# Kernel tuning notes

Hardware: AMD Instinct MI355X
Metric: run time of the kernel (lower is better)

The kernel has to match this reference:

```python
import jax, jax.numpy as jnp
import numpy as np
import math

NUM_BUCKETS = 32
MAX_DISTANCE = 128
N_HEADS = 16
D_KV = 64


def _relative_position_bucket(relative_position, num_buckets=NUM_BUCKETS, max_distance=MAX_DISTANCE):
    # bidirectional (encoder) variant
    num_buckets //= 2
    relative_buckets = (relative_position > 0).astype(jnp.int32) * num_buckets
    rp = jnp.abs(relative_position)
    max_exact = num_buckets // 2
    is_small = rp < max_exact
    rp_large = max_exact + (
        jnp.log(jnp.maximum(rp, 1).astype(jnp.float32) / max_exact)
        / math.log(max_distance / max_exact)
        * (num_buckets - max_exact)
    ).astype(jnp.int32)
    rp_large = jnp.minimum(rp_large, num_buckets - 1)
    return relative_buckets + jnp.where(is_small, rp, rp_large)


def compute_bias(rel_bias, q_len, k_len):
    ctx = jnp.arange(q_len)[:, None]
    mem = jnp.arange(k_len)[None, :]
    buckets = _relative_position_bucket(mem - ctx)          # [q, k]
    values = rel_bias[buckets]                               # [q, k, h]
    return jnp.transpose(values, (2, 0, 1))[None]            # [1, h, q, k]


def setup_inputs() -> dict:
    key = jax.random.key(0)
    ks = jax.random.split(key, 6)
    d_model, inner = 1024, N_HEADS * D_KV
    s = 0.02
    return {
        "hidden_states": jax.random.normal(ks[0], (2, 2048, d_model), jnp.float32),
        "Wq": jax.random.normal(ks[1], (d_model, inner), jnp.float32) * s,
        "Wk": jax.random.normal(ks[2], (d_model, inner), jnp.float32) * s,
        "Wv": jax.random.normal(ks[3], (d_model, inner), jnp.float32) * s,
        "Wo": jax.random.normal(ks[4], (inner, d_model), jnp.float32) * s,
        "rel_bias": jax.random.normal(ks[5], (NUM_BUCKETS, N_HEADS), jnp.float32) * s,
    }


def reference(hidden_states, Wq, Wk, Wv, Wo, rel_bias):
    B, S, D = hidden_states.shape

    def split_heads(x):  # [B,S,inner] -> [B,H,S,dk]
        return x.reshape(B, S, N_HEADS, D_KV).transpose(0, 2, 1, 3)

    q = split_heads(hidden_states @ Wq)
    k = split_heads(hidden_states @ Wk)
    v = split_heads(hidden_states @ Wv)

    # T5 does NOT scale by 1/sqrt(d_kv)
    scores = jnp.einsum("bhqd,bhkd->bhqk", q, k)
    scores = scores + compute_bias(rel_bias, S, S)
    attn = jax.nn.softmax(scores, axis=-1)
    ctx = jnp.einsum("bhqk,bhkd->bhqd", attn, v)
    ctx = ctx.transpose(0, 2, 1, 3).reshape(B, S, N_HEADS * D_KV)
    return ctx @ Wo
```

## Files before the change

kernel.cpp:

```cpp
#include <hip/hip_runtime.h>
#include <hip/hip_bf16.h>

typedef __bf16 bf16x8 __attribute__((ext_vector_type(8)));
typedef __bf16 bf16x4 __attribute__((ext_vector_type(4)));
typedef float floatx4 __attribute__((ext_vector_type(4)));
typedef float floatx16 __attribute__((ext_vector_type(16)));
using bf16 = __hip_bfloat16;

#define S_    2048
#define NHEAD 16
#define LOG2E 1.4426950408889634f

__device__ __forceinline__ void load_lds16(const bf16* g, void* lds) {
  __builtin_amdgcn_global_load_lds((const __attribute__((address_space(1))) void*)g,
                                   (__attribute__((address_space(3))) void*)lds, 16, 0, 0);
}

__global__ void prep_kernel(const float* __restrict__ hidden,
                            const float* __restrict__ wq, const float* __restrict__ wk,
                            const float* __restrict__ wv, const float* __restrict__ wo,
                            const float* __restrict__ rel_bias,
                            bf16* __restrict__ hbf, bf16* __restrict__ wt_qkv,
                            bf16* __restrict__ wt_o, float* __restrict__ tab) {
  __shared__ bf16 tile[32][33];
  int bid = blockIdx.x;
  if (bid < 4096) {
    int i = (bid * 256 + threadIdx.x) * 4;
    float4 v = *(const float4*)(hidden + i);
    bf16 o[4] = {__float2bfloat16(v.x), __float2bfloat16(v.y),
                 __float2bfloat16(v.z), __float2bfloat16(v.w)};
    *(uint2*)(hbf + i) = *(const uint2*)o;
  } else if (bid < 8192) {
    int r = bid - 4096;
    int mat = r >> 10;
    int rem = r & 1023;
    int n0 = (rem & 31) * 32, k0 = (rem >> 5) * 32;
    int tx = threadIdx.x & 31, ty = threadIdx.x >> 5;
    const float* src = (mat == 0) ? wq : (mat == 1) ? wk : (mat == 2) ? wv : wo;
    bf16* dst = (mat == 3) ? wt_o : wt_qkv + mat * 1024 * 1024;
#pragma unroll
    for (int j = 0; j < 32; j += 8)
      tile[ty + j][tx] = __float2bfloat16(src[(k0 + ty + j) * 1024 + n0 + tx]);
    __syncthreads();
#pragma unroll
    for (int j = 0; j < 32; j += 8)
      dst[(n0 + ty + j) * 1024 + k0 + tx] = tile[tx][ty + j];
  } else {
    int idx = (bid - 8192) * 256 + threadIdx.x;
    int h = idx >> 12, j = idx & 4095;
    int delta = j - 2048;
    int rb = (delta > 0) ? 16 : 0;
    int rpa = delta < 0 ? -delta : delta;
    int bsmall;
    if (rpa < 8) {
      bsmall = rpa;
    } else {
      int lg = 25 - __clz(rpa * rpa);
      bsmall = 8 + lg;
      if (bsmall > 15) bsmall = 15;
    }
    tab[idx] = rel_bias[(rb + bsmall) * 16 + h] * LOG2E;
  }
}

__global__ __launch_bounds__(512) void gemm_qkv_kernel(const bf16* __restrict__ A,
                                                       const bf16* __restrict__ Bt,
                                                       bf16* __restrict__ qh,
                                                       bf16* __restrict__ kf,
                                                       bf16* __restrict__ vf) {
  const int K = 1024;
  __shared__ char lds[131072];
  int t = threadIdx.x;
  int m0 = blockIdx.y * 256, n0 = blockIdx.x * 256;
  int w = t >> 6, lane = t & 63, ln = lane & 15, quad = lane >> 4;
  int wm = w >> 2, wn = w & 3;
  floatx4 acc[8][4];
  floatx4 zero = {0.f, 0.f, 0.f, 0.f};
#pragma unroll
  for (int i = 0; i < 8; i++)
#pragma unroll
    for (int j = 0; j < 4; j++) acc[i][j] = zero;

  int r = t >> 3, c8 = t & 7;
  int cs = (c8 ^ (r & 7)) * 8;
  const bf16* Ag = A + (long)(m0 + r) * K + cs;
  const bf16* Bg = Bt + (long)(n0 + r) * K + cs;

#define QKV_STAGE(bufi, kt)                                                     \
  {                                                                             \
    char* ab = lds + (bufi) * 65536;                                            \
    char* bb = ab + 32768;                                                      \
    int kk = (kt) * 64;                                                         \
    _Pragma("unroll")                                                           \
    for (int ch = 0; ch < 4; ch++) {                                            \
      load_lds16(Ag + (long)ch * 64 * K + kk, ab + ch * 8192 + t * 16);         \
      load_lds16(Bg + (long)ch * 64 * K + kk, bb + ch * 8192 + t * 16);         \
    }                                                                           \
  }

  QKV_STAGE(0, 0);
  QKV_STAGE(1, 1);
  asm volatile("s_waitcnt vmcnt(8)" ::: "memory");
  __builtin_amdgcn_s_barrier();

  for (int kt = 0; kt < 16; ++kt) {
    const bf16* As_ = (const bf16*)(lds + (kt & 1) * 65536);
    const bf16* Bs_ = As_ + 16384;
#pragma unroll
    for (int s = 0; s < 2; s++) {
      int slot = ((s * 4 + quad) ^ (ln & 7)) * 8;
      bf16x8 af[8], bfv[4];
#pragma unroll
      for (int i = 0; i < 8; i++)
        af[i] = *(const bf16x8*)&As_[(wm * 128 + i * 16 + ln) * 64 + slot];
#pragma unroll
      for (int j = 0; j < 4; j++)
        bfv[j] = *(const bf16x8*)&Bs_[(wn * 64 + j * 16 + ln) * 64 + slot];
      __builtin_amdgcn_s_setprio(1);
#pragma unroll
      for (int i = 0; i < 8; i++)
#pragma unroll
        for (int j = 0; j < 4; j++)
          acc[i][j] = __builtin_amdgcn_mfma_f32_16x16x32_bf16(af[i], bfv[j], acc[i][j], 0, 0, 0);
      __builtin_amdgcn_s_setprio(0);
    }
    if (kt == 15) break;
    __builtin_amdgcn_s_barrier();
    if (kt + 2 < 16) {
      QKV_STAGE(kt & 1, kt + 2);
      asm volatile("s_waitcnt vmcnt(8)" ::: "memory");
    } else {
      asm volatile("s_waitcnt vmcnt(0)" ::: "memory");
    }
    __builtin_amdgcn_s_barrier();
  }
#undef QKV_STAGE

  int nb = n0 + wn * 64;
  int type = nb >> 10, h = (nb >> 6) & 15;
  int b = (m0 >> 11);
  int sl0 = (m0 & 2047) + wm * 128;
  long bhbase = (long)((b * 16 + h)) * 131072;

  if (type == 0) {
#pragma unroll
    for (int i = 0; i < 8; i++)
#pragma unroll
      for (int j = 0; j < 4; j++) {
        int d = j * 16 + ln;
#pragma unroll
        for (int rr = 0; rr < 4; rr++) {
          int s = sl0 + i * 16 + quad * 4 + rr;
          qh[bhbase + (long)s * 64 + d] = __float2bfloat16(acc[i][j][rr]);
        }
      }
  } else if (type == 1) {
#pragma unroll
    for (int i = 0; i < 8; i++)
#pragma unroll
      for (int j = 0; j < 4; j++) {
        long base = bhbase + sl0 * 64 + (i >> 1) * 2048 + j * 512 + (ln >> 3) * 256 +
                    (i & 1) * 128 + quad * 32 + (ln & 7);
#pragma unroll
        for (int rr = 0; rr < 4; rr++)
          kf[base + rr * 8] = __float2bfloat16(acc[i][j][rr]);
      }
  } else {
#pragma unroll
    for (int i = 0; i < 8; i++)
#pragma unroll
      for (int j = 0; j < 4; j++) {
        long off = sl0 * 64 + i * 1024 + (j >> 1) * 512 + (quad >> 1) * 256 +
                   ((j & 1) * 16 + ln) * 8 + (quad & 1) * 4;
        bf16x4 pk = {(__bf16)acc[i][j][0], (__bf16)acc[i][j][1],
                     (__bf16)acc[i][j][2], (__bf16)acc[i][j][3]};
        *(bf16x4*)(vf + bhbase + off) = pk;
      }
  }
}

#define LOADKV(Kr, Vr, kk)                                        \
  {                                                               \
    const bf16* kp = kfb + (kk) * 64 + loff;                      \
    const bf16* vp = vfb + (kk) * 64 + loff;                      \
    Kr[0] = *(const bf16x8*)(kp);                                 \
    Kr[1] = *(const bf16x8*)(kp + 512);                           \
    Kr[2] = *(const bf16x8*)(kp + 1024);                          \
    Kr[3] = *(const bf16x8*)(kp + 1536);                          \
    Vr[0] = *(const bf16x8*)(vp);                                 \
    Vr[1] = *(const bf16x8*)(vp + 512);                           \
    Vr[2] = *(const bf16x8*)(vp + 1024);                          \
    Vr[3] = *(const bf16x8*)(vp + 1536);                          \
  }

#define COMPUTE(Kr, Vr, kk)                                                       \
  {                                                                               \
    floatx16 st = zf;                                                             \
    __builtin_amdgcn_s_setprio(1);                                                \
    st = __builtin_amdgcn_mfma_f32_32x32x16_bf16(Kr[0], Qf[0], st, 0, 0, 0);      \
    st = __builtin_amdgcn_mfma_f32_32x32x16_bf16(Kr[1], Qf[1], st, 0, 0, 0);      \
    st = __builtin_amdgcn_mfma_f32_32x32x16_bf16(Kr[2], Qf[2], st, 0, 0, 0);      \
    st = __builtin_amdgcn_mfma_f32_32x32x16_bf16(Kr[3], Qf[3], st, 0, 0, 0);      \
    __builtin_amdgcn_s_setprio(0);                                                \
    float p[16];                                                                  \
    bool near = ((kk) > qw - 160) && ((kk) < qw + 160);                           \
    if (near) {                                                                   \
      int kb = (kk) + 4 * h5 - (qw + l31) + 2048;                                 \
      _Pragma("unroll")                                                           \
      for (int r = 0; r < 16; r++)                                                \
        p[r] = __builtin_amdgcn_exp2f(                                            \
            fmaf(st[r], LOG2E, bt[kb + (r & 3) + 8 * (r >> 2)]));                 \
    } else {                                                                      \
      float cb = ((kk) > qw) ? cpos : cneg;                                       \
      _Pragma("unroll")                                                           \
      for (int r = 0; r < 16; r++)                                                \
        p[r] = __builtin_amdgcn_exp2f(fmaf(st[r], LOG2E, cb));                    \
    }                                                                             \
    float a0 = (p[0] + p[1]) + (p[2] + p[3]);                                     \
    float a1 = (p[4] + p[5]) + (p[6] + p[7]);                                     \
    float a2 = (p[8] + p[9]) + (p[10] + p[11]);                                   \
    float a3 = (p[12] + p[13]) + (p[14] + p[15]);                                 \
    l_acc += (a0 + a1) + (a2 + a3);                                               \
    unsigned d[8];                                                                \
    _Pragma("unroll")                                                             \
    for (int i = 0; i < 8; i++)                                                   \
      asm("v_cvt_pk_bf16_f32 %0, %1, %2" : "=v"(d[i]) : "v"(p[2*i]), "v"(p[2*i+1])); \
    unsigned w0 = d[0], w2 = d[2];                                                \
    asm("v_permlane32_swap_b32 %0, %1" : "+v"(w0), "+v"(w2));                     \
    unsigned w1 = d[1], w3 = d[3];                                                \
    asm("v_permlane32_swap_b32 %0, %1" : "+v"(w1), "+v"(w3));                     \
    unsigned w4 = d[4], w6 = d[6];                                                \
    asm("v_permlane32_swap_b32 %0, %1" : "+v"(w4), "+v"(w6));                     \
    unsigned w5 = d[5], w7 = d[7];                                                \
    asm("v_permlane32_swap_b32 %0, %1" : "+v"(w5), "+v"(w7));                     \
    union { unsigned u[4]; bf16x8 v; } a0u, a1u;                                  \
    a0u.u[0] = w0; a0u.u[1] = w1; a0u.u[2] = w2; a0u.u[3] = w3;                   \
    a1u.u[0] = w4; a1u.u[1] = w5; a1u.u[2] = w6; a1u.u[3] = w7;                   \
    __builtin_amdgcn_s_setprio(1);                                                \
    o0 = __builtin_amdgcn_mfma_f32_32x32x16_bf16(a0u.v, Vr[0], o0, 0, 0, 0);      \
    o1 = __builtin_amdgcn_mfma_f32_32x32x16_bf16(a0u.v, Vr[1], o1, 0, 0, 0);      \
    o0 = __builtin_amdgcn_mfma_f32_32x32x16_bf16(a1u.v, Vr[2], o0, 0, 0, 0);      \
    o1 = __builtin_amdgcn_mfma_f32_32x32x16_bf16(a1u.v, Vr[3], o1, 0, 0, 0);      \
    __builtin_amdgcn_s_setprio(0);                                                \
  }

__global__ __launch_bounds__(256, 2) void attn_kernel(const bf16* __restrict__ qh,
                                                      const bf16* __restrict__ kf,
                                                      const bf16* __restrict__ vf,
                                                      const float* __restrict__ btab,
                                                      bf16* __restrict__ ctx) {
  int t = threadIdx.x, w = t >> 6, lane = t & 63;
  int l31 = lane & 31, h5 = lane >> 5;

  int lin = blockIdx.x;
  int xcd = lin & 7, j = lin >> 3;
  int bh = xcd * 4 + (j >> 4);
  int qblk = j & 15;
  int b = bh >> 4, h = bh & 15;
  int qw = qblk * 128 + w * 32;

  const bf16* qbase = qh + (long)bh * S_ * 64;
  const bf16* kfb = kf + (long)bh * S_ * 64;
  const bf16* vfb = vf + (long)bh * S_ * 64;
  const float* bt = btab + h * 4096;
  int loff = h5 * 256 + l31 * 8;

  bf16x8 Qf[4];
#pragma unroll
  for (int ds = 0; ds < 4; ds++)
    Qf[ds] = *(const bf16x8*)(qbase + (long)(qw + l31) * 64 + ds * 16 + h5 * 8);

  float cneg = bt[0], cpos = bt[4095];
  float l_acc = 0.f;
  floatx16 zf = {0.f, 0.f, 0.f, 0.f, 0.f, 0.f, 0.f, 0.f,
                 0.f, 0.f, 0.f, 0.f, 0.f, 0.f, 0.f, 0.f};
  floatx16 o0 = zf, o1 = zf;

  bf16x8 Ka[4], Va[4], Kb[4], Vb[4];
  LOADKV(Ka, Va, 0);
  LOADKV(Kb, Vb, 32);

  for (int k0 = 0; k0 < S_; k0 += 64) {
    COMPUTE(Ka, Va, k0);
    if (k0 + 64 < S_) LOADKV(Ka, Va, k0 + 64);
    COMPUTE(Kb, Vb, k0 + 32);
    if (k0 + 96 < S_) LOADKV(Kb, Vb, k0 + 96);
  }

  l_acc += __shfl_xor(l_acc, 32);
  float linv = 1.0f / l_acc;
#pragma unroll
  for (int r = 0; r < 16; r++) {
    int qrow = (r & 3) + 8 * (r >> 2) + 4 * h5;
    float lv = __shfl(linv, qrow);
    int q = qw + qrow;
    long base = (long)(b * S_ + q) * 1024 + h * 64 + l31;
    ctx[base] = __float2bfloat16(o0[r] * lv);
    ctx[base + 32] = __float2bfloat16(o1[r] * lv);
  }
}

__global__ __launch_bounds__(256) void gemm_bt_kernel(const bf16* __restrict__ A,
                                                      const bf16* __restrict__ Bt,
                                                      float* __restrict__ C,
                                                      int M, int N, int K) {
  __shared__ bf16 As[64 * 32];
  __shared__ bf16 Bs[128 * 32];
  int t = threadIdx.x;
  int m0 = blockIdx.y * 64, n0 = blockIdx.x * 128;
  int w = t >> 6, lane = t & 63, ln = lane & 15, quad = lane >> 4;
  int wr = w & 1, wc = w >> 1;
  floatx4 acc[2][4];
  floatx4 zero = {0.f, 0.f, 0.f, 0.f};
#pragma unroll
  for (int i = 0; i < 2; i++)
#pragma unroll
    for (int j = 0; j < 4; j++) acc[i][j] = zero;

  int r = t >> 2, c = (t & 3) * 8;
  const bf16* Ag = A + (long)(m0 + r) * K + c;
  const bf16* Bg = Bt + (long)(n0 + r) * K + c;
  char* ldsA0 = (char*)As + w * 1024;
  char* ldsB0 = (char*)Bs + w * 1024;
  char* ldsB1 = ldsB0 + 4096;

  for (int k0 = 0; k0 < K; k0 += 32) {
    load_lds16(Ag + k0, ldsA0);
    load_lds16(Bg + k0, ldsB0);
    load_lds16(Bg + (long)64 * K + k0, ldsB1);
    __syncthreads();
    bf16x8 af[2], bfv[4];
#pragma unroll
    for (int i = 0; i < 2; i++)
      af[i] = *(const bf16x8*)&As[(wr * 32 + i * 16 + ln) * 32 + quad * 8];
#pragma unroll
    for (int j = 0; j < 4; j++)
      bfv[j] = *(const bf16x8*)&Bs[(wc * 64 + j * 16 + ln) * 32 + quad * 8];
#pragma unroll
    for (int i = 0; i < 2; i++)
#pragma unroll
      for (int j = 0; j < 4; j++)
        acc[i][j] = __builtin_amdgcn_mfma_f32_16x16x32_bf16(af[i], bfv[j], acc[i][j], 0, 0, 0);
    __syncthreads();
  }

#pragma unroll
  for (int i = 0; i < 2; i++)
#pragma unroll
    for (int j = 0; j < 4; j++)
#pragma unroll
      for (int rr = 0; rr < 4; rr++)
        C[(long)(m0 + wr * 32 + i * 16 + quad * 4 + rr) * N + n0 + wc * 64 + j * 16 + ln] =
            acc[i][j][rr];
}

extern "C" void kernel_launch(void* const* d_in, const int* in_sizes, int n_in,
                              void* d_out, int out_size, void* d_ws, size_t ws_size,
                              hipStream_t stream) {
  (void)in_sizes; (void)n_in; (void)out_size; (void)ws_size;
  const float* hidden   = (const float*)d_in[0];
  const float* Wq       = (const float*)d_in[1];
  const float* Wk       = (const float*)d_in[2];
  const float* Wv       = (const float*)d_in[3];
  const float* Wo       = (const float*)d_in[4];
  const float* rel_bias = (const float*)d_in[5];

  char* ws = (char*)d_ws;
  bf16*  hbf    = (bf16*)(ws + 0);
  bf16*  wt_qkv = (bf16*)(ws + 8388608);
  bf16*  wt_o   = (bf16*)(ws + 14680064);
  float* btab   = (float*)(ws + 16777216);
  bf16*  qh     = (bf16*)(ws + 17039360);
  bf16*  kf     = (bf16*)(ws + 25427968);
  bf16*  vf     = (bf16*)(ws + 33816576);
  bf16*  ctx    = (bf16*)(ws + 42205184);

  prep_kernel<<<dim3(8448), dim3(256), 0, stream>>>(hidden, Wq, Wk, Wv, Wo, rel_bias,
                                                    hbf, wt_qkv, wt_o, btab);
  gemm_qkv_kernel<<<dim3(12, 16), dim3(512), 0, stream>>>(hbf, wt_qkv, qh, kf, vf);
  attn_kernel<<<dim3(512), dim3(256), 0, stream>>>(qh, kf, vf, btab, ctx);
  gemm_bt_kernel<<<dim3(8, 64), dim3(256), 0, stream>>>(ctx, wt_o, (float*)d_out, 4096, 1024, 1024);
}
```

Before: 187.8 us.

## Double-buffer output GEMM loads, enlarge weight transpose tiles, reuse workspace for ctx

```diff
diff --git a/kernel.cpp b/kernel.cpp
--- a/kernel.cpp
+++ b/kernel.cpp
@@ -22,7 +22,7 @@
                             const float* __restrict__ rel_bias,
                             bf16* __restrict__ hbf, bf16* __restrict__ wt_qkv,
                             bf16* __restrict__ wt_o, float* __restrict__ tab) {
-  __shared__ bf16 tile[32][33];
+  __shared__ bf16 tile[64][65];
   int bid = blockIdx.x;
   if (bid < 4096) {
     int i = (bid * 256 + threadIdx.x) * 4;
@@ -30,23 +30,23 @@
     bf16 o[4] = {__float2bfloat16(v.x), __float2bfloat16(v.y),
                  __float2bfloat16(v.z), __float2bfloat16(v.w)};
     *(uint2*)(hbf + i) = *(const uint2*)o;
-  } else if (bid < 8192) {
+  } else if (bid < 5120) {
     int r = bid - 4096;
-    int mat = r >> 10;
-    int rem = r & 1023;
-    int n0 = (rem & 31) * 32, k0 = (rem >> 5) * 32;
-    int tx = threadIdx.x & 31, ty = threadIdx.x >> 5;
+    int mat = r >> 8;
+    int rem = r & 255;
+    int n0 = (rem & 15) * 64, k0 = (rem >> 4) * 64;
+    int tx = threadIdx.x & 63, ty = threadIdx.x >> 6;
     const float* src = (mat == 0) ? wq : (mat == 1) ? wk : (mat == 2) ? wv : wo;
     bf16* dst = (mat == 3) ? wt_o : wt_qkv + mat * 1024 * 1024;
 #pragma unroll
-    for (int j = 0; j < 32; j += 8)
+    for (int j = 0; j < 64; j += 4)
       tile[ty + j][tx] = __float2bfloat16(src[(k0 + ty + j) * 1024 + n0 + tx]);
     __syncthreads();
 #pragma unroll
-    for (int j = 0; j < 32; j += 8)
+    for (int j = 0; j < 64; j += 4)
       dst[(n0 + ty + j) * 1024 + k0 + tx] = tile[tx][ty + j];
   } else {
-    int idx = (bid - 8192) * 256 + threadIdx.x;
+    int idx = (bid - 5120) * 256 + threadIdx.x;
     int h = idx >> 12, j = idx & 4095;
     int delta = j - 2048;
     int rb = (delta > 0) ? 16 : 0;
@@ -304,8 +304,7 @@
                                                       const bf16* __restrict__ Bt,
                                                       float* __restrict__ C,
                                                       int M, int N, int K) {
-  __shared__ bf16 As[64 * 32];
-  __shared__ bf16 Bs[128 * 32];
+  __shared__ char lds[2][12288];
   int t = threadIdx.x;
   int m0 = blockIdx.y * 64, n0 = blockIdx.x * 128;
   int w = t >> 6, lane = t & 63, ln = lane & 15, quad = lane >> 4;
@@ -320,29 +319,49 @@
   int r = t >> 2, c = (t & 3) * 8;
   const bf16* Ag = A + (long)(m0 + r) * K + c;
   const bf16* Bg = Bt + (long)(n0 + r) * K + c;
-  char* ldsA0 = (char*)As + w * 1024;
-  char* ldsB0 = (char*)Bs + w * 1024;
-  char* ldsB1 = ldsB0 + 4096;
-
-  for (int k0 = 0; k0 < K; k0 += 32) {
-    load_lds16(Ag + k0, ldsA0);
-    load_lds16(Bg + k0, ldsB0);
-    load_lds16(Bg + (long)64 * K + k0, ldsB1);
-    __syncthreads();
+
+#define BT_STAGE(bufi, kt)                                                      \
+  {                                                                             \
+    int kk = (kt) * 32;                                                         \
+    char* base = lds[bufi] + w * 1024;                                          \
+    load_lds16(Ag + kk, base);                                                  \
+    load_lds16(Bg + kk, base + 4096);                                           \
+    load_lds16(Bg + (long)64 * K + kk, base + 8192);                            \
+  }
+
+  BT_STAGE(0, 0);
+  BT_STAGE(1, 1);
+  asm volatile("s_waitcnt vmcnt(3)" ::: "memory");
+  __builtin_amdgcn_s_barrier();
+
+  for (int kt = 0; kt < 32; ++kt) {
+    const bf16* As_ = (const bf16*)lds[kt & 1];
+    const bf16* Bs_ = As_ + 2048;
     bf16x8 af[2], bfv[4];
 #pragma unroll
     for (int i = 0; i < 2; i++)
-      af[i] = *(const bf16x8*)&As[(wr * 32 + i * 16 + ln) * 32 + quad * 8];
+      af[i] = *(const bf16x8*)&As_[(wr * 32 + i * 16 + ln) * 32 + quad * 8];
 #pragma unroll
     for (int j = 0; j < 4; j++)
-      bfv[j] = *(const bf16x8*)&Bs[(wc * 64 + j * 16 + ln) * 32 + quad * 8];
+      bfv[j] = *(const bf16x8*)&Bs_[(wc * 64 + j * 16 + ln) * 32 + quad * 8];
+    __builtin_amdgcn_s_setprio(1);
 #pragma unroll
     for (int i = 0; i < 2; i++)
 #pragma unroll
       for (int j = 0; j < 4; j++)
         acc[i][j] = __builtin_amdgcn_mfma_f32_16x16x32_bf16(af[i], bfv[j], acc[i][j], 0, 0, 0);
-    __syncthreads();
-  }
+    __builtin_amdgcn_s_setprio(0);
+    if (kt == 31) break;
+    __builtin_amdgcn_s_barrier();
+    if (kt + 2 < 32) {
+      BT_STAGE(kt & 1, kt + 2);
+      asm volatile("s_waitcnt vmcnt(3)" ::: "memory");
+    } else {
+      asm volatile("s_waitcnt vmcnt(0)" ::: "memory");
+    }
+    __builtin_amdgcn_s_barrier();
+  }
+#undef BT_STAGE
 
 #pragma unroll
   for (int i = 0; i < 2; i++)
@@ -373,9 +392,9 @@
   bf16*  qh     = (bf16*)(ws + 17039360);
   bf16*  kf     = (bf16*)(ws + 25427968);
   bf16*  vf     = (bf16*)(ws + 33816576);
-  bf16*  ctx    = (bf16*)(ws + 42205184);
-
-  prep_kernel<<<dim3(8448), dim3(256), 0, stream>>>(hidden, Wq, Wk, Wv, Wo, rel_bias,
+  bf16*  ctx    = hbf;
+
+  prep_kernel<<<dim3(5376), dim3(256), 0, stream>>>(hidden, Wq, Wk, Wv, Wo, rel_bias,
                                                     hbf, wt_qkv, wt_o, btab);
   gemm_qkv_kernel<<<dim3(12, 16), dim3(512), 0, stream>>>(hbf, wt_qkv, qh, kf, vf);
   attn_kernel<<<dim3(512), dim3(256), 0, stream>>>(qh, kf, vf, btab, ctx);
```

Measured after the change: 185.8 us. Within noise of the previous version (-1.1%).
